# Optimization experiments

Hardware: AMD Instinct MI355X
Metric: run time of the kernel (lower is better)

## Reference

```python
import jax, jax.numpy as jnp
import numpy as np

NUM_HEADS = 8
GRAPH_DIM = 64
K_RATIO = 0.1
SIM_THRESH = 0.6


def _gat_layer(h_in, mask, W, a_src, a_dst, b):
    # PyG GATConv (heads=1, eval mode): lin (no bias), alpha = LeakyReLU(a_src.h_j + a_dst.h_i),
    # softmax over source nodes j per target i (edges given by dense mask, self loops included), + bias.
    h = h_in @ W                                   # [N, F]
    asrc = h @ a_src                               # [N] source term
    adst = h @ a_dst                               # [N] target term
    logits = jax.nn.leaky_relu(adst[:, None] + asrc[None, :], 0.2)  # [target i, source j]
    logits = jnp.where(mask.T, logits, -1e30)      # mask[j,i]: edge src j -> dst i (symmetric here)
    alpha = jax.nn.softmax(logits, axis=-1)
    return alpha @ h + b


def _forward(x, w_qkv, w_proj, b_proj, gat0_W, gat0_asrc, gat0_adst, gat0_b,
             gat1_W, gat1_asrc, gat1_adst, gat1_b, w_g2a, b_g2a):
    B, C, H, W = x.shape
    HW = H * W
    nh = NUM_HEADS
    hd = C // nh
    scale = hd ** -0.5
    x_seq = x.reshape(B, C, HW).transpose(0, 2, 1)                 # [B, HW, C]

    # ---- build_spatial_graph ----
    importance = jnp.var(x_seq, axis=-1, ddof=1)                   # torch.var default unbiased
    N = int(HW * K_RATIO)                                          # 102 nodes
    _, top_idx = jax.lax.top_k(importance, N)                      # [B, N]
    feats = jnp.take_along_axis(x_seq, top_idx[..., None], axis=1) # [B, N, C]
    fn = feats / jnp.clip(jnp.linalg.norm(feats, axis=-1, keepdims=True), 1e-12)
    sim = fn @ fn.transpose(0, 2, 1)                               # [B, N, N]
    adj = sim > SIM_THRESH
    adj = adj | jnp.eye(N, dtype=bool)                             # GATConv add_self_loops

    # ---- per-batch GAT stack + graph_to_attn ----
    def per_graph(f, m):
        g = jax.nn.relu(_gat_layer(f, m, gat0_W, gat0_asrc, gat0_adst, gat0_b))
        g = jax.nn.relu(_gat_layer(g, m, gat1_W, gat1_asrc, gat1_adst, gat1_b))
        return jax.nn.sigmoid(g @ w_g2a.T + b_g2a)                 # [N, nh]
    gw = jax.vmap(per_graph)(feats, adj)                           # [B, N, nh]

    # ---- dense multi-head attention ----
    qkv = (x_seq @ w_qkv.T).reshape(B, HW, 3, nh, hd).transpose(2, 0, 3, 1, 4)
    q, k, v = qkv[0], qkv[1], qkv[2]                               # [B, nh, HW, hd]
    scores = jnp.einsum('bhqd,bhkd->bhqk', q, k) * scale           # [B, nh, HW, HW]

    # ---- graph modulation scatter (replaces the nested python loops) ----
    vals = jnp.where(adj[..., None], gw[:, :, None, :] * gw[:, None, :, :], 0.0)  # [B, N, N, nh]
    gm = jnp.zeros_like(scores)
    bidx = jnp.arange(B)[:, None, None]
    gm = gm.at[bidx, :, top_idx[:, :, None], top_idx[:, None, :]].set(vals)
    scores = scores + gm

    attn = jax.nn.softmax(scores, axis=-1)                         # dropout is identity in eval
    out = jnp.einsum('bhqk,bhkd->bhqd', attn, v).transpose(0, 2, 1, 3).reshape(B, HW, C)
    out = out @ w_proj.T + b_proj
    return out.transpose(0, 2, 1).reshape(B, C, H, W)


def setup_inputs() -> dict:
    key = jax.random.key(0)
    ks = jax.random.split(key, 16)
    dim, gd, nh = 256, GRAPH_DIM, NUM_HEADS
    B, H, W = 8, 32, 32
    s = 0.02
    return {
        'x': jax.random.normal(ks[0], (B, dim, H, W), dtype=jnp.float32),
        'w_qkv': s * jax.random.normal(ks[1], (3 * dim, dim), dtype=jnp.float32),
        'w_proj': s * jax.random.normal(ks[2], (dim, dim), dtype=jnp.float32),
        'b_proj': jnp.zeros((dim,), dtype=jnp.float32),
        'gat0_W': s * jax.random.normal(ks[3], (dim, gd), dtype=jnp.float32),
        'gat0_asrc': s * jax.random.normal(ks[4], (gd,), dtype=jnp.float32),
        'gat0_adst': s * jax.random.normal(ks[5], (gd,), dtype=jnp.float32),
        'gat0_b': jnp.zeros((gd,), dtype=jnp.float32),
        'gat1_W': s * jax.random.normal(ks[6], (gd, gd), dtype=jnp.float32),
        'gat1_asrc': s * jax.random.normal(ks[7], (gd,), dtype=jnp.float32),
        'gat1_adst': s * jax.random.normal(ks[8], (gd,), dtype=jnp.float32),
        'gat1_b': jnp.zeros((gd,), dtype=jnp.float32),
        'w_g2a': s * jax.random.normal(ks[9], (nh, gd), dtype=jnp.float32),
        'b_g2a': jnp.zeros((nh,), dtype=jnp.float32),
    }


def reference(x, w_qkv, w_proj, b_proj, gat0_W, gat0_asrc, gat0_adst, gat0_b,
              gat1_W, gat1_asrc, gat1_adst, gat1_b, w_g2a, b_g2a):
    return _forward(x, w_qkv, w_proj, b_proj, gat0_W, gat0_asrc, gat0_adst, gat0_b,
                    gat1_W, gat1_asrc, gat1_adst, gat1_b, w_g2a, b_g2a)
```

## Files before the change

### kernel.cpp

```cpp
#include <hip/hip_runtime.h>
#include <math.h>

#define NB 8
#define CDIM 256
#define HWD 1024
#define NH 8
#define HD 32
#define NN 102
#define GD 64

typedef __attribute__((ext_vector_type(8))) short bf16x8;
typedef __attribute__((ext_vector_type(4))) float f32x4;

__device__ inline short f2bf(float f) {
  union { float f; unsigned u; } v; v.f = f;
  unsigned r = v.u + 0x7fffu + ((v.u >> 16) & 1u);
  return (short)(r >> 16);
}
__device__ inline float bf2f(short s) {
  union { unsigned u; float f; } v;
  v.u = ((unsigned)(unsigned short)s) << 16;
  return v.f;
}

__global__ __launch_bounds__(256) void wsplit_k(const float* __restrict__ w_qkv,
                                                const float* __restrict__ w_proj,
                                                short* __restrict__ wqh, short* __restrict__ wql,
                                                short* __restrict__ wph, short* __restrict__ wpl) {
  int t = blockIdx.x * 256 + threadIdx.x;
  if (t < 196608) {
    float v = w_qkv[t];
    short hi = f2bf(v);
    wqh[t] = hi; wql[t] = f2bf(v - bf2f(hi));
  } else {
    int u = t - 196608;
    float v = w_proj[u];
    short hi = f2bf(v);
    wph[u] = hi; wpl[u] = f2bf(v - bf2f(hi));
  }
}

__global__ __launch_bounds__(256) void xsplit_k(const float* __restrict__ x,
                                                short* __restrict__ xth,
                                                short* __restrict__ xtl) {
  __shared__ float tile[64][65];
  int p0 = blockIdx.x * 64, c0 = blockIdx.y * 64, b = blockIdx.z;
  int t = threadIdx.x;
  {
    int g = t >> 6, p = t & 63;
#pragma unroll
    for (int i = 0; i < 16; ++i) {
      int cc = g * 16 + i;
      tile[cc][p] = x[((size_t)(b * 256 + c0 + cc)) * 1024 + p0 + p];
    }
  }
  __syncthreads();
  {
    int p = t >> 2, cs = (t & 3) * 16;
    size_t rb = ((size_t)(b * 1024 + p0 + p)) * 256 + c0 + cs;
#pragma unroll
    for (int g = 0; g < 4; ++g) {
      short4 hv, lv;
      float f0 = tile[cs + g * 4 + 0][p];
      float f1 = tile[cs + g * 4 + 1][p];
      float f2 = tile[cs + g * 4 + 2][p];
      float f3 = tile[cs + g * 4 + 3][p];
      hv.x = f2bf(f0); lv.x = f2bf(f0 - bf2f(hv.x));
      hv.y = f2bf(f1); lv.y = f2bf(f1 - bf2f(hv.y));
      hv.z = f2bf(f2); lv.z = f2bf(f2 - bf2f(hv.z));
      hv.w = f2bf(f3); lv.w = f2bf(f3 - bf2f(hv.w));
      *(short4*)(xth + rb + g * 4) = hv;
      *(short4*)(xtl + rb + g * 4) = lv;
    }
  }
}

__global__ __launch_bounds__(256) void prep_k(const float* __restrict__ g0W,
                                              const float* __restrict__ g1W,
                                              short* __restrict__ w0bT,
                                              short* __restrict__ w1bT) {
  int t = blockIdx.x * 256 + threadIdx.x;
  if (t < 16384) {
    int c = t >> 6, f = t & 63;
    w0bT[f * 256 + c] = f2bf(g0W[t]);
  } else if (t < 20480) {
    int u2 = t - 16384;
    int c = u2 >> 6, f = u2 & 63;
    w1bT[f * 64 + c] = f2bf(g1W[u2]);
  }
}

__global__ __launch_bounds__(256) void importance_k(const float* __restrict__ x,
                                                    float* __restrict__ imp) {
  __shared__ float red[8][33];
  int bp = blockIdx.x;
  int b = bp >> 5, p0 = (bp & 31) << 5;
  int t = threadIdx.x;
  int pl = t & 31, cg = t >> 5;
  const float* xp = x + (size_t)b * CDIM * HWD + p0 + pl;
  float s = 0.f;
  for (int cc = 0; cc < 32; ++cc) s += xp[(size_t)(cg * 32 + cc) * HWD];
  red[cg][pl] = s;
  __syncthreads();
  float tot = 0.f;
  for (int g = 0; g < 8; ++g) tot += red[g][pl];
  float mean = tot * (1.f / CDIM);
  __syncthreads();
  float v = 0.f;
  for (int cc = 0; cc < 32; ++cc) {
    float d = xp[(size_t)(cg * 32 + cc) * HWD] - mean;
    v += d * d;
  }
  red[cg][pl] = v;
  __syncthreads();
  if (t < 32) {
    float vv = 0.f;
    for (int g = 0; g < 8; ++g) vv += red[g][t];
    imp[b * 1024 + p0 + t] = vv * (1.f / (CDIM - 1));
  }
}

union GraphLDS {
  struct { float sv[1024]; int si[1024]; } tk;
  struct {
    short h0T[64 * 136];
    short alphaB[102 * 136];
    short gB[102 * 72];
  } m;
};

__global__ __launch_bounds__(1024) void graph_k(
    const float* __restrict__ x, const float* __restrict__ imp,
    const short* __restrict__ w0bT, const short* __restrict__ w1bT,
    const float* __restrict__ g0as, const float* __restrict__ g0ad,
    const float* __restrict__ g0b,
    const float* __restrict__ g1as, const float* __restrict__ g1ad,
    const float* __restrict__ g1b,
    const float* __restrict__ wg2a, const float* __restrict__ bg2a,
    int* __restrict__ nodeof, short* __restrict__ fnG,
    unsigned char* __restrict__ adjG, float* __restrict__ gwb) {
  __shared__ GraphLDS u;
  __shared__ ushort adjPack[NN][8];
  __shared__ float normL[NN];
  __shared__ float asrcL[NN], adstL[NN];
  __shared__ int topiL[NN];
  int b = blockIdx.x, t = threadIdx.x;
  int wv = t >> 6, lane = t & 63, quad = lane >> 4, l16 = lane & 15;

  u.tk.sv[t] = imp[b * 1024 + t];
  u.tk.si[t] = t;
  nodeof[b * 1024 + t] = -1;
  __syncthreads();
  for (int k = 2; k <= 1024; k <<= 1) {
    for (int j = k >> 1; j > 0; j >>= 1) {
      int ixj = t ^ j;
      if (ixj > t) {
        bool up = ((t & k) == 0);
        float a = u.tk.sv[t], c = u.tk.sv[ixj];
        if ((a > c) == up) {
          u.tk.sv[t] = c; u.tk.sv[ixj] = a;
          int ti = u.tk.si[t]; u.tk.si[t] = u.tk.si[ixj]; u.tk.si[ixj] = ti;
        }
      }
      __syncthreads();
    }
  }
  if (t >= 1024 - NN) {
    int n = 1023 - t;
    int idx = u.tk.si[t];
    topiL[n] = idx;
    nodeof[b * 1024 + idx] = n;
  }
  __syncthreads();

  {
    int n = t >> 3, g = t & 7;
    if (n < NN) {
      int idx = topiL[n];
      const float* xb = x + (size_t)b * CDIM * HWD + idx;
      float vbuf[32];
      float ssl = 0.f;
#pragma unroll
      for (int cc = 0; cc < 32; ++cc) {
        float v = xb[(size_t)(g * 32 + cc) * HWD];
        vbuf[cc] = v;
        ssl += v * v;
      }
      ssl += __shfl_xor(ssl, 1);
      ssl += __shfl_xor(ssl, 2);
      ssl += __shfl_xor(ssl, 4);
      float nrm = sqrtf(ssl);
      float rn = 1.f / fmaxf(nrm, 1e-12f);
      if (g == 0) normL[n] = nrm;
      short* fp = fnG + ((size_t)b * 112 + n) * 256 + g * 32;
#pragma unroll
      for (int cc = 0; cc < 32; cc += 4) {
        short4 s4 = {f2bf(vbuf[cc] * rn), f2bf(vbuf[cc + 1] * rn),
                     f2bf(vbuf[cc + 2] * rn), f2bf(vbuf[cc + 3] * rn)};
        *(short4*)(fp + cc) = s4;
      }
    }
  }
  for (int e = t; e < 64 * 34; e += 1024) {
    int f = e / 34, c = 102 + (e % 34);
    u.m.h0T[f * 136 + c] = 0;
  }
  __syncthreads();

  for (int tile = wv; tile < 49; tile += 16) {
    int I = tile / 7, J = tile % 7;
    const short* ap = fnG + ((size_t)b * 112 + I * 16 + l16) * 256 + quad * 8;
    const short* bp = fnG + ((size_t)b * 112 + J * 16 + l16) * 256 + quad * 8;
    f32x4 acc = (f32x4){0.f, 0.f, 0.f, 0.f};
#pragma unroll
    for (int kb = 0; kb < 8; ++kb)
      acc = __builtin_amdgcn_mfma_f32_16x16x32_bf16(*(const bf16x8*)(ap + kb * 32),
                                                    *(const bf16x8*)(bp + kb * 32), acc, 0, 0, 0);
#pragma unroll
    for (int r = 0; r < 4; ++r) {
      int i = I * 16 + quad * 4 + r, j = J * 16 + l16;
      bool e = (acc[r] > 0.6f) || (i == j);
      unsigned long long m = __ballot(e);
      if (l16 == 0) {
        int row = I * 16 + quad * 4 + r;
        if (row < NN) adjPack[row][J] = (ushort)((m >> (quad * 16)) & 0xFFFFull);
      }
      if (i < NN && j < NN) adjG[(size_t)b * NN * NN + i * NN + j] = e ? 1 : 0;
    }
  }
  __syncthreads();

  for (int tile = wv; tile < 28; tile += 16) {
    int mt = tile >> 2, nt = tile & 3;
    const short* ap = fnG + ((size_t)b * 112 + mt * 16 + l16) * 256 + quad * 8;
    const short* bp = w0bT + (nt * 16 + l16) * 256 + quad * 8;
    f32x4 acc = (f32x4){0.f, 0.f, 0.f, 0.f};
#pragma unroll
    for (int kb = 0; kb < 8; ++kb)
      acc = __builtin_amdgcn_mfma_f32_16x16x32_bf16(*(const bf16x8*)(ap + kb * 32),
                                                    *(const bf16x8*)(bp + kb * 32), acc, 0, 0, 0);
    int f = nt * 16 + l16;
#pragma unroll
    for (int r = 0; r < 4; ++r) {
      int node = mt * 16 + quad * 4 + r;
      if (node < NN) u.m.h0T[f * 136 + node] = f2bf(acc[r] * normL[node]);
    }
  }
  __syncthreads();

  for (int layer = 0; layer < 2; ++layer) {
    const float* avs = layer ? g1as : g0as;
    const float* avd = layer ? g1ad : g0ad;
    const float* bias = layer ? g1b : g0b;
    {
      int n = t >> 3, g = t & 7;
      if (n < NN) {
        float s1 = 0.f, s2 = 0.f;
#pragma unroll
        for (int uu = 0; uu < 8; ++uu) {
          int f = g * 8 + uu;
          float hv = bf2f(u.m.h0T[f * 136 + n]);
          s1 += hv * avs[f];
          s2 += hv * avd[f];
        }
        s1 += __shfl_xor(s1, 1); s1 += __shfl_xor(s1, 2); s1 += __shfl_xor(s1, 4);
        s2 += __shfl_xor(s2, 1); s2 += __shfl_xor(s2, 2); s2 += __shfl_xor(s2, 4);
        if (g == 0) { asrcL[n] = s1; adstL[n] = s2; }
      }
    }
    __syncthreads();
    for (int i = wv; i < NN; i += 16) {
      float zi = adstL[i];
      int j1 = 64 + lane;
      bool e0 = (adjPack[i][lane >> 4] >> (lane & 15)) & 1;
      bool e1 = (j1 < NN) && ((adjPack[i][j1 >> 4] >> (j1 & 15)) & 1);
      float p0 = 0.f, p1 = 0.f;
      if (e0) { float z = zi + asrcL[lane]; p0 = __expf(z > 0.f ? z : 0.2f * z); }
      if (e1) { float z = zi + asrcL[j1]; p1 = __expf(z > 0.f ? z : 0.2f * z); }
      float s = p0 + p1;
      s += __shfl_xor(s, 1); s += __shfl_xor(s, 2); s += __shfl_xor(s, 4);
      s += __shfl_xor(s, 8); s += __shfl_xor(s, 16); s += __shfl_xor(s, 32);
      float inv = 1.f / s;
      u.m.alphaB[i * 136 + lane] = f2bf(p0 * inv);
      u.m.alphaB[i * 136 + 64 + lane] = f2bf(p1 * inv);
    }
    __syncthreads();
    for (int tile = wv; tile < 28; tile += 16) {
      int mt = tile >> 2, nt = tile & 3;
      int ar = mt * 16 + l16; if (ar > NN - 1) ar = NN - 1;
      const short* ap = &u.m.alphaB[ar * 136 + quad * 8];
      const short* bp = &u.m.h0T[(nt * 16 + l16) * 136 + quad * 8];
      f32x4 acc = (f32x4){0.f, 0.f, 0.f, 0.f};
#pragma unroll
      for (int kb = 0; kb < 4; ++kb)
        acc = __builtin_amdgcn_mfma_f32_16x16x32_bf16(*(const bf16x8*)(ap + kb * 32),
                                                      *(const bf16x8*)(bp + kb * 32), acc, 0, 0, 0);
      int f = nt * 16 + l16;
      float bv = bias[f];
#pragma unroll
      for (int r = 0; r < 4; ++r) {
        int i = mt * 16 + quad * 4 + r;
        if (i < NN) u.m.gB[i * 72 + f] = f2bf(fmaxf(acc[r] + bv, 0.f));
      }
    }
    __syncthreads();
    if (layer == 0) {
      for (int tile = wv; tile < 28; tile += 16) {
        int mt = tile >> 2, nt = tile & 3;
        int ar = mt * 16 + l16; if (ar > NN - 1) ar = NN - 1;
        const short* ap = &u.m.gB[ar * 72 + quad * 8];
        const short* bp = w1bT + (nt * 16 + l16) * 64 + quad * 8;
        f32x4 acc = (f32x4){0.f, 0.f, 0.f, 0.f};
#pragma unroll
        for (int kb = 0; kb < 2; ++kb)
          acc = __builtin_amdgcn_mfma_f32_16x16x32_bf16(*(const bf16x8*)(ap + kb * 32),
                                                        *(const bf16x8*)(bp + kb * 32), acc, 0, 0, 0);
        int f = nt * 16 + l16;
#pragma unroll
        for (int r = 0; r < 4; ++r) {
          int node = mt * 16 + quad * 4 + r;
          if (node < NN) u.m.h0T[f * 136 + node] = f2bf(acc[r]);
        }
      }
      __syncthreads();
    }
  }
  float* wgL = (float*)&u.m.alphaB[0];
  if (t < 512) wgL[t] = wg2a[t];
  __syncthreads();
  if (t < NN * NH) {
    int n = t >> 3, h = t & 7;
    float z = bg2a[h];
#pragma unroll
    for (int c = 0; c < GD; ++c) z += bf2f(u.m.gB[n * 72 + c]) * wgL[h * 64 + c];
    gwb[((size_t)b * NN + n) * NH + h] = 1.f / (1.f + __expf(-z));
  }
}

__global__ __launch_bounds__(256) void qkv_k(const short* __restrict__ xth,
                                             const short* __restrict__ xtl,
                                             const short* __restrict__ wqh,
                                             const short* __restrict__ wql,
                                             short* __restrict__ qhp, short* __restrict__ qlp,
                                             short* __restrict__ khp, short* __restrict__ klp,
                                             short* __restrict__ vtp) {
  __shared__ short vs_s[4][64 * 24];
  int t = threadIdx.x, wid = t >> 6, lane = t & 63, quad = lane >> 4, l16 = lane & 15;
  int m0 = blockIdx.x * 64, y = blockIdx.y;
  int b = m0 >> 10;
  int row = m0 + wid * 16 + l16;
  int p_base = (m0 & 1023) + wid * 16;
  int qi = y >> 2, n0 = (y & 3) * 64;
  const short* wh = wqh + (size_t)(qi * 256 + n0) * 256;
  const short* wl = wql + (size_t)(qi * 256 + n0) * 256;
  const short* arh = xth + (size_t)row * 256 + quad * 8;
  const short* arl = xtl + (size_t)row * 256 + quad * 8;
  f32x4 acc[4];
#pragma unroll
  for (int nt = 0; nt < 4; ++nt) acc[nt] = (f32x4){0.f, 0.f, 0.f, 0.f};
#pragma unroll
  for (int kb = 0; kb < 8; ++kb) {
    bf16x8 ah = *(const bf16x8*)(arh + kb * 32);
    bf16x8 al = *(const bf16x8*)(arl + kb * 32);
#pragma unroll
    for (int nt = 0; nt < 4; ++nt) {
      size_t wo = (size_t)(nt * 16 + l16) * 256 + kb * 32 + quad * 8;
      bf16x8 bh_ = *(const bf16x8*)(wh + wo);
      bf16x8 bl_ = *(const bf16x8*)(wl + wo);
      acc[nt] = __builtin_amdgcn_mfma_f32_16x16x32_bf16(ah, bh_, acc[nt], 0, 0, 0);
      acc[nt] = __builtin_amdgcn_mfma_f32_16x16x32_bf16(ah, bl_, acc[nt], 0, 0, 0);
      acc[nt] = __builtin_amdgcn_mfma_f32_16x16x32_bf16(al, bh_, acc[nt], 0, 0, 0);
    }
  }
  if (qi < 2) {
    const float scale = (qi == 0) ? 0.17677669529663687f : 1.f;
    short* hp = (qi == 0) ? qhp : khp;
    short* lp = (qi == 0) ? qlp : klp;
#pragma unroll
    for (int nt = 0; nt < 4; ++nt) {
      int nq = n0 + nt * 16 + l16;
      int h = nq >> 5, d = nq & 31;
#pragma unroll
      for (int r = 0; r < 4; ++r) {
        int p = p_base + quad * 4 + r;
        float v = acc[nt][r] * scale;
        short hi = f2bf(v);
        short lo = f2bf(v - bf2f(hi));
        size_t e = ((size_t)(b * 8 + h) * 1024 + p) * 32 + d;
        hp[e] = hi;
        lp[e] = lo;
      }
    }
  } else {
    short* vs = &vs_s[wid][0];
#pragma unroll
    for (int nt = 0; nt < 4; ++nt)
#pragma unroll
      for (int r = 0; r < 4; ++r)
        vs[(nt * 16 + l16) * 24 + quad * 4 + r] = f2bf(acc[nt][r]);
    int nq = n0 + lane;
    int h = nq >> 5, d = nq & 31;
    size_t rb = ((size_t)(b * 8 + h) * 32 + d) * 1024 + p_base;
    *(bf16x8*)(vtp + rb) = *(const bf16x8*)(vs + lane * 24);
    *(bf16x8*)(vtp + rb + 8) = *(const bf16x8*)(vs + lane * 24 + 8);
  }
}

__global__ __launch_bounds__(256, 4) void attn_k(const short* __restrict__ qh,
                                                 const short* __restrict__ ql,
                                                 const short* __restrict__ kh,
                                                 const short* __restrict__ kl,
                                                 const short* __restrict__ vt,
                                                 const int* __restrict__ nodeof,
                                                 const float* __restrict__ gw,
                                                 const unsigned char* __restrict__ adj,
                                                 short* __restrict__ aoh,
                                                 short* __restrict__ aol) {
  __shared__ __align__(16) short p_s[4][16 * 72];
  __shared__ float aw_s[4][16];
  int t = threadIdx.x;
  int wid = t >> 6, lane = t & 63, quad = lane >> 4, l16 = lane & 15;
  int bh = blockIdx.x, b = bh >> 3, h = bh & 7;
  int q0 = blockIdx.y * 64 + wid * 16;
  size_t base = (size_t)bh * 32768;
  short* pw = &p_s[wid][0];
  float* aw = &aw_s[wid][0];

  size_t qoff = base + (size_t)(q0 + l16) * 32 + quad * 8;
  bf16x8 qhf = *(const bf16x8*)(qh + qoff);
  bf16x8 qlf = *(const bf16x8*)(ql + qoff);

  int irow[4]; float grq[4];
#pragma unroll
  for (int r = 0; r < 4; ++r) {
    int qr = q0 + quad * 4 + r;
    int in_ = nodeof[b * 1024 + qr];
    irow[r] = in_;
    grq[r] = (in_ >= 0) ? gw[((size_t)b * NN + in_) * NH + h] : 0.f;
  }
  const unsigned char* adjB = adj + (size_t)b * NN * NN;

  f32x4 ot[2];
  ot[0] = (f32x4){0.f, 0.f, 0.f, 0.f};
  ot[1] = (f32x4){0.f, 0.f, 0.f, 0.f};
  float l_r[4] = {0.f, 0.f, 0.f, 0.f};

  for (int ch = 0; ch < 16; ++ch) {
    int c0 = ch * 64;
    bf16x8 khf[4], klf[4];
#pragma unroll
    for (int ni = 0; ni < 4; ++ni) {
      size_t off = base + (size_t)(c0 + ni * 16 + l16) * 32 + quad * 8;
      khf[ni] = *(const bf16x8*)(kh + off);
      klf[ni] = *(const bf16x8*)(kl + off);
    }
    bf16x8 vaf[2][2];
#pragma unroll
    for (int mi = 0; mi < 2; ++mi)
#pragma unroll
      for (int ks = 0; ks < 2; ++ks)
        vaf[mi][ks] = *(const bf16x8*)(vt + base + (size_t)(mi * 16 + l16) * 1024 +
                                       c0 + ks * 32 + quad * 8);
    int jn[4]; float gcn[4];
#pragma unroll
    for (int ni = 0; ni < 4; ++ni) {
      int j = nodeof[b * 1024 + c0 + ni * 16 + l16];
      jn[ni] = j;
      gcn[ni] = (j >= 0) ? gw[((size_t)b * NN + j) * NH + h] : 0.f;
    }
    f32x4 s[4];
#pragma unroll
    for (int ni = 0; ni < 4; ++ni) {
      f32x4 a = (f32x4){0.f, 0.f, 0.f, 0.f};
      a = __builtin_amdgcn_mfma_f32_16x16x32_bf16(qhf, khf[ni], a, 0, 0, 0);
      a = __builtin_amdgcn_mfma_f32_16x16x32_bf16(qhf, klf[ni], a, 0, 0, 0);
      a = __builtin_amdgcn_mfma_f32_16x16x32_bf16(qlf, khf[ni], a, 0, 0, 0);
      s[ni] = a;
    }
#pragma unroll
    for (int r = 0; r < 4; ++r) {
      int in_ = irow[r];
      if (in_ >= 0) {
        const unsigned char* ar = adjB + (size_t)in_ * NN;
        float g = grq[r];
#pragma unroll
        for (int ni = 0; ni < 4; ++ni)
          if (jn[ni] >= 0 && ar[jn[ni]]) s[ni][r] += g * gcn[ni];
      }
    }
#pragma unroll
    for (int r = 0; r < 4; ++r) {
      float e0 = __expf(s[0][r]);
      float e1 = __expf(s[1][r]);
      float e2 = __expf(s[2][r]);
      float e3 = __expf(s[3][r]);
      l_r[r] += (e0 + e1) + (e2 + e3);
      int prow = (quad * 4 + r) * 72;
      pw[prow + 0 + l16] = f2bf(e0);
      pw[prow + 16 + l16] = f2bf(e1);
      pw[prow + 32 + l16] = f2bf(e2);
      pw[prow + 48 + l16] = f2bf(e3);
    }
#pragma unroll
    for (int ks = 0; ks < 2; ++ks) {
      bf16x8 pb = *(const bf16x8*)(pw + l16 * 72 + ks * 32 + quad * 8);
      ot[0] = __builtin_amdgcn_mfma_f32_16x16x32_bf16(vaf[0][ks], pb, ot[0], 0, 0, 0);
      ot[1] = __builtin_amdgcn_mfma_f32_16x16x32_bf16(vaf[1][ks], pb, ot[1], 0, 0, 0);
    }
  }
#pragma unroll
  for (int r = 0; r < 4; ++r) {
    float ls = l_r[r];
    ls += __shfl_xor(ls, 1);
    ls += __shfl_xor(ls, 2);
    ls += __shfl_xor(ls, 4);
    ls += __shfl_xor(ls, 8);
    if (l16 == 0) aw[quad * 4 + r] = 1.f / ls;
  }
  float li = aw[l16];
  ot[0] *= li;
  ot[1] *= li;
  float* os = (float*)pw;
#pragma unroll
  for (int mi = 0; mi < 2; ++mi)
#pragma unroll
    for (int r = 0; r < 4; ++r)
      os[l16 * 36 + mi * 16 + quad * 4 + r] = ot[mi][r];
  int qr2 = lane >> 2, dg = (lane & 3) * 8;
  float f[8];
  *(float4*)&f[0] = *(float4*)&os[qr2 * 36 + dg];
  *(float4*)&f[4] = *(float4*)&os[qr2 * 36 + dg + 4];
  bf16x8 hv, lv;
#pragma unroll
  for (int j = 0; j < 8; ++j) {
    hv[j] = f2bf(f[j]);
    lv[j] = f2bf(f[j] - bf2f(hv[j]));
  }
  size_t ob = (size_t)(b * 1024 + q0 + qr2) * 256 + h * 32 + dg;
  *(bf16x8*)(aoh + ob) = hv;
  *(bf16x8*)(aol + ob) = lv;
}

__global__ __launch_bounds__(256) void proj_k(const short* __restrict__ aoh,
                                              const short* __restrict__ aol,
                                              const short* __restrict__ wph,
                                              const short* __restrict__ wpl,
                                              const float* __restrict__ bias,
                                              float* __restrict__ out) {
  __shared__ float os_s[4][64 * 20];
  int t = threadIdx.x, wid = t >> 6, lane = t & 63, quad = lane >> 4, l16 = lane & 15;
  int m0 = blockIdx.x * 64, n0 = blockIdx.y * 64;
  int b = m0 >> 10;
  int row = m0 + wid * 16 + l16;
  int p_base = (m0 & 1023) + wid * 16;
  const short* arh = aoh + (size_t)row * 256 + quad * 8;
  const short* arl = aol + (size_t)row * 256 + quad * 8;
  f32x4 acc[4];
#pragma unroll
  for (int nt = 0; nt < 4; ++nt) acc[nt] = (f32x4){0.f, 0.f, 0.f, 0.f};
#pragma unroll
  for (int kb = 0; kb < 8; ++kb) {
    bf16x8 ah = *(const bf16x8*)(arh + kb * 32);
    bf16x8 al = *(const bf16x8*)(arl + kb * 32);
#pragma unroll
    for (int nt = 0; nt < 4; ++nt) {
      size_t wo = (size_t)(n0 + nt * 16 + l16) * 256 + kb * 32 + quad * 8;
      bf16x8 bh_ = *(const bf16x8*)(wph + wo);
      bf16x8 bl_ = *(const bf16x8*)(wpl + wo);
      acc[nt] = __builtin_amdgcn_mfma_f32_16x16x32_bf16(ah, bh_, acc[nt], 0, 0, 0);
      acc[nt] = __builtin_amdgcn_mfma_f32_16x16x32_bf16(ah, bl_, acc[nt], 0, 0, 0);
      acc[nt] = __builtin_amdgcn_mfma_f32_16x16x32_bf16(al, bh_, acc[nt], 0, 0, 0);
    }
  }
  float* os = &os_s[wid][0];
#pragma unroll
  for (int nt = 0; nt < 4; ++nt) {
    float bv = bias[n0 + nt * 16 + l16];
#pragma unroll
    for (int r = 0; r < 4; ++r)
      os[(nt * 16 + l16) * 20 + quad * 4 + r] = acc[nt][r] + bv;
  }
  int c = n0 + lane;
  float* orow = out + ((size_t)(b * 256 + c)) * 1024 + p_base;
#pragma unroll
  for (int g = 0; g < 4; ++g)
    *(float4*)(orow + g * 4) = *(float4*)&os[lane * 20 + g * 4];
}

extern "C" void kernel_launch(void* const* d_in, const int* in_sizes, int n_in,
                              void* d_out, int out_size, void* d_ws, size_t ws_size,
                              hipStream_t stream) {
  const float* x      = (const float*)d_in[0];
  const float* w_qkv  = (const float*)d_in[1];
  const float* w_proj = (const float*)d_in[2];
  const float* b_proj = (const float*)d_in[3];
  const float* g0W    = (const float*)d_in[4];
  const float* g0as   = (const float*)d_in[5];
  const float* g0ad   = (const float*)d_in[6];
  const float* g0b    = (const float*)d_in[7];
  const float* g1W    = (const float*)d_in[8];
  const float* g1as   = (const float*)d_in[9];
  const float* g1ad   = (const float*)d_in[10];
  const float* g1b    = (const float*)d_in[11];
  const float* wg2a   = (const float*)d_in[12];
  const float* bg2a   = (const float*)d_in[13];
  float* out = (float*)d_out;
  float* ws = (float*)d_ws;

  size_t o = 0;
  auto alloc = [&](size_t nf) { float* p = ws + o; o += (nf + 15) & ~(size_t)15; return p; };
  float* imp    = alloc(8 * 1024);
  int*   nodeof = (int*)alloc(8 * 1024);
  short* fnG    = (short*)alloc(8 * 112 * 256 / 2);
  short* w0bT   = (short*)alloc(256 * 64 / 2);
  short* w1bT   = (short*)alloc(64 * 64 / 2);
  unsigned char* adj = (unsigned char*)alloc((8 * NN * NN + 3) / 4 + 16);
  float* gwb    = alloc(8 * NN * 8);
  short* xth    = (short*)alloc(1048576);
  short* xtl    = (short*)alloc(1048576);
  short* wqh    = (short*)alloc(98304);
  short* wql    = (short*)alloc(98304);
  short* wph    = (short*)alloc(32768);
  short* wpl    = (short*)alloc(32768);
  short* qh     = (short*)alloc(1048576);
  short* ql     = (short*)alloc(1048576);
  short* kh     = (short*)alloc(1048576);
  short* kl     = (short*)alloc(1048576);
  short* vt     = (short*)alloc(1048576);
  short* aoh    = (short*)alloc(1048576);
  short* aol    = (short*)alloc(1048576);
  if (ws_size < o * sizeof(float)) return;

  importance_k<<<256, 256, 0, stream>>>(x, imp);
  wsplit_k<<<1024, 256, 0, stream>>>(w_qkv, w_proj, wqh, wql, wph, wpl);
  xsplit_k<<<dim3(16, 4, 8), 256, 0, stream>>>(x, xth, xtl);
  prep_k<<<80, 256, 0, stream>>>(g0W, g1W, w0bT, w1bT);
  graph_k<<<8, 1024, 0, stream>>>(x, imp, w0bT, w1bT, g0as, g0ad, g0b,
                                  g1as, g1ad, g1b, wg2a, bg2a,
                                  nodeof, fnG, adj, gwb);
  qkv_k<<<dim3(128, 12), 256, 0, stream>>>(xth, xtl, wqh, wql, qh, ql, kh, kl, vt);
  attn_k<<<dim3(64, 16), 256, 0, stream>>>(qh, ql, kh, kl, vt, nodeof, gwb, adj, aoh, aol);
  proj_k<<<dim3(128, 4), 256, 0, stream>>>(aoh, aol, wph, wpl, b_proj, out);
}
```

Baseline: 356.1 us.

## Split attention over key halves with a reduce pass, halve GEMM output tiles

The attention kernel now splits each query tile's key range into two halves on a third grid dimension. Each half writes unnormalized partial outputs and row sums to fp32 scratch, and a new reduce kernel combines them, normalizes, and produces the hi/lo bf16 split. The QKV and projection GEMMs use 32-wide output tiles instead of 64-wide, doubling block count, and several kernels get a higher occupancy launch bound. The goal is more blocks to fill the GPU, at the cost of an extra launch, scratch traffic, and less reuse of the A operand in the GEMMs.

```diff
diff --git a/kernel.cpp b/kernel.cpp
--- a/kernel.cpp
+++ b/kernel.cpp
@@ -337,33 +337,33 @@
   }
 }
 
-__global__ __launch_bounds__(256) void qkv_k(const short* __restrict__ xth,
-                                             const short* __restrict__ xtl,
-                                             const short* __restrict__ wqh,
-                                             const short* __restrict__ wql,
-                                             short* __restrict__ qhp, short* __restrict__ qlp,
-                                             short* __restrict__ khp, short* __restrict__ klp,
-                                             short* __restrict__ vtp) {
-  __shared__ short vs_s[4][64 * 24];
+__global__ __launch_bounds__(256, 8) void qkv_k(const short* __restrict__ xth,
+                                                const short* __restrict__ xtl,
+                                                const short* __restrict__ wqh,
+                                                const short* __restrict__ wql,
+                                                short* __restrict__ qhp, short* __restrict__ qlp,
+                                                short* __restrict__ khp, short* __restrict__ klp,
+                                                short* __restrict__ vtp) {
+  __shared__ short vs_s[4][32 * 24];
   int t = threadIdx.x, wid = t >> 6, lane = t & 63, quad = lane >> 4, l16 = lane & 15;
   int m0 = blockIdx.x * 64, y = blockIdx.y;
   int b = m0 >> 10;
   int row = m0 + wid * 16 + l16;
   int p_base = (m0 & 1023) + wid * 16;
-  int qi = y >> 2, n0 = (y & 3) * 64;
-  const short* wh = wqh + (size_t)(qi * 256 + n0) * 256;
-  const short* wl = wql + (size_t)(qi * 256 + n0) * 256;
+  int qi = y >> 3, n0 = (y & 7) * 32;
+  const short* wh = wqh + ((size_t)qi * 256 + n0) * 256;
+  const short* wl = wql + ((size_t)qi * 256 + n0) * 256;
   const short* arh = xth + (size_t)row * 256 + quad * 8;
   const short* arl = xtl + (size_t)row * 256 + quad * 8;
-  f32x4 acc[4];
-#pragma unroll
-  for (int nt = 0; nt < 4; ++nt) acc[nt] = (f32x4){0.f, 0.f, 0.f, 0.f};
+  f32x4 acc[2];
+  acc[0] = (f32x4){0.f, 0.f, 0.f, 0.f};
+  acc[1] = (f32x4){0.f, 0.f, 0.f, 0.f};
 #pragma unroll
   for (int kb = 0; kb < 8; ++kb) {
     bf16x8 ah = *(const bf16x8*)(arh + kb * 32);
     bf16x8 al = *(const bf16x8*)(arl + kb * 32);
 #pragma unroll
-    for (int nt = 0; nt < 4; ++nt) {
+    for (int nt = 0; nt < 2; ++nt) {
       size_t wo = (size_t)(nt * 16 + l16) * 256 + kb * 32 + quad * 8;
       bf16x8 bh_ = *(const bf16x8*)(wh + wo);
       bf16x8 bl_ = *(const bf16x8*)(wl + wo);
@@ -377,7 +377,7 @@
     short* hp = (qi == 0) ? qhp : khp;
     short* lp = (qi == 0) ? qlp : klp;
 #pragma unroll
-    for (int nt = 0; nt < 4; ++nt) {
+    for (int nt = 0; nt < 2; ++nt) {
       int nq = n0 + nt * 16 + l16;
       int h = nq >> 5, d = nq & 31;
 #pragma unroll
@@ -394,19 +394,19 @@
   } else {
     short* vs = &vs_s[wid][0];
 #pragma unroll
-    for (int nt = 0; nt < 4; ++nt)
+    for (int nt = 0; nt < 2; ++nt)
 #pragma unroll
       for (int r = 0; r < 4; ++r)
         vs[(nt * 16 + l16) * 24 + quad * 4 + r] = f2bf(acc[nt][r]);
-    int nq = n0 + lane;
+    int cl = lane >> 1, hf = lane & 1;
+    int nq = n0 + cl;
     int h = nq >> 5, d = nq & 31;
-    size_t rb = ((size_t)(b * 8 + h) * 32 + d) * 1024 + p_base;
-    *(bf16x8*)(vtp + rb) = *(const bf16x8*)(vs + lane * 24);
-    *(bf16x8*)(vtp + rb + 8) = *(const bf16x8*)(vs + lane * 24 + 8);
-  }
-}
-
-__global__ __launch_bounds__(256, 4) void attn_k(const short* __restrict__ qh,
+    size_t rb = ((size_t)(b * 8 + h) * 32 + d) * 1024 + p_base + hf * 8;
+    *(bf16x8*)(vtp + rb) = *(const bf16x8*)(vs + cl * 24 + hf * 8);
+  }
+}
+
+__global__ __launch_bounds__(256, 8) void attn_k(const short* __restrict__ qh,
                                                  const short* __restrict__ ql,
                                                  const short* __restrict__ kh,
                                                  const short* __restrict__ kl,
@@ -414,14 +414,15 @@
                                                  const int* __restrict__ nodeof,
                                                  const float* __restrict__ gw,
                                                  const unsigned char* __restrict__ adj,
-                                                 short* __restrict__ aoh,
-                                                 short* __restrict__ aol) {
+                                                 float* __restrict__ po,
+                                                 float* __restrict__ pl) {
   __shared__ __align__(16) short p_s[4][16 * 72];
   __shared__ float aw_s[4][16];
   int t = threadIdx.x;
   int wid = t >> 6, lane = t & 63, quad = lane >> 4, l16 = lane & 15;
   int bh = blockIdx.x, b = bh >> 3, h = bh & 7;
-  int q0 = blockIdx.y * 64 + wid * 16;
+  int qt = blockIdx.y, khalf = blockIdx.z;
+  int q0 = qt * 64 + wid * 16;
   size_t base = (size_t)bh * 32768;
   short* pw = &p_s[wid][0];
   float* aw = &aw_s[wid][0];
@@ -445,7 +446,7 @@
   ot[1] = (f32x4){0.f, 0.f, 0.f, 0.f};
   float l_r[4] = {0.f, 0.f, 0.f, 0.f};
 
-  for (int ch = 0; ch < 16; ++ch) {
+  for (int ch = khalf * 8; ch < khalf * 8 + 8; ++ch) {
     int c0 = ch * 64;
     bf16x8 khf[4], klf[4];
 #pragma unroll
@@ -515,55 +516,77 @@
     ls += __shfl_xor(ls, 2);
     ls += __shfl_xor(ls, 4);
     ls += __shfl_xor(ls, 8);
-    if (l16 == 0) aw[quad * 4 + r] = 1.f / ls;
-  }
-  float li = aw[l16];
-  ot[0] *= li;
-  ot[1] *= li;
+    if (l16 == 0) aw[quad * 4 + r] = ls;
+  }
   float* os = (float*)pw;
 #pragma unroll
   for (int mi = 0; mi < 2; ++mi)
 #pragma unroll
     for (int r = 0; r < 4; ++r)
       os[l16 * 36 + mi * 16 + quad * 4 + r] = ot[mi][r];
+  int bht = bh * 16 + qt;
+  size_t pob = (((size_t)bht * 2 + khalf) * 64 + wid * 16) * 32;
   int qr2 = lane >> 2, dg = (lane & 3) * 8;
-  float f[8];
-  *(float4*)&f[0] = *(float4*)&os[qr2 * 36 + dg];
-  *(float4*)&f[4] = *(float4*)&os[qr2 * 36 + dg + 4];
+  *(float4*)&po[pob + qr2 * 32 + dg] = *(float4*)&os[qr2 * 36 + dg];
+  *(float4*)&po[pob + qr2 * 32 + dg + 4] = *(float4*)&os[qr2 * 36 + dg + 4];
+  if (lane < 16) pl[((size_t)bht * 2 + khalf) * 64 + wid * 16 + lane] = aw[lane];
+}
+
+__global__ __launch_bounds__(256) void reduce_k(const float* __restrict__ po,
+                                                const float* __restrict__ pl,
+                                                short* __restrict__ aoh,
+                                                short* __restrict__ aol) {
+  int bht = blockIdx.x;
+  int bh = bht >> 4, qt = bht & 15;
+  int b = bh >> 3, h = bh & 7;
+  int t = threadIdx.x;
+  int q = t >> 2, dg = (t & 3) * 8;
+  size_t b0 = (((size_t)bht * 2 + 0) * 64 + q) * 32 + dg;
+  size_t b1 = (((size_t)bht * 2 + 1) * 64 + q) * 32 + dg;
+  float4 a0 = *(const float4*)&po[b0];
+  float4 a1 = *(const float4*)&po[b0 + 4];
+  float4 c0 = *(const float4*)&po[b1];
+  float4 c1 = *(const float4*)&po[b1 + 4];
+  float l = pl[((size_t)bht * 2) * 64 + q] + pl[((size_t)bht * 2 + 1) * 64 + q];
+  float inv = 1.f / l;
+  float f[8] = {(a0.x + c0.x) * inv, (a0.y + c0.y) * inv,
+                (a0.z + c0.z) * inv, (a0.w + c0.w) * inv,
+                (a1.x + c1.x) * inv, (a1.y + c1.y) * inv,
+                (a1.z + c1.z) * inv, (a1.w + c1.w) * inv};
   bf16x8 hv, lv;
 #pragma unroll
   for (int j = 0; j < 8; ++j) {
     hv[j] = f2bf(f[j]);
     lv[j] = f2bf(f[j] - bf2f(hv[j]));
   }
-  size_t ob = (size_t)(b * 1024 + q0 + qr2) * 256 + h * 32 + dg;
+  size_t ob = (size_t)(b * 1024 + qt * 64 + q) * 256 + h * 32 + dg;
   *(bf16x8*)(aoh + ob) = hv;
   *(bf16x8*)(aol + ob) = lv;
 }
 
-__global__ __launch_bounds__(256) void proj_k(const short* __restrict__ aoh,
-                                              const short* __restrict__ aol,
-                                              const short* __restrict__ wph,
-                                              const short* __restrict__ wpl,
-                                              const float* __restrict__ bias,
-                                              float* __restrict__ out) {
-  __shared__ float os_s[4][64 * 20];
+__global__ __launch_bounds__(256, 8) void proj_k(const short* __restrict__ aoh,
+                                                 const short* __restrict__ aol,
+                                                 const short* __restrict__ wph,
+                                                 const short* __restrict__ wpl,
+                                                 const float* __restrict__ bias,
+                                                 float* __restrict__ out) {
+  __shared__ float os_s[4][32 * 20];
   int t = threadIdx.x, wid = t >> 6, lane = t & 63, quad = lane >> 4, l16 = lane & 15;
-  int m0 = blockIdx.x * 64, n0 = blockIdx.y * 64;
+  int m0 = blockIdx.x * 64, n0 = blockIdx.y * 32;
   int b = m0 >> 10;
   int row = m0 + wid * 16 + l16;
   int p_base = (m0 & 1023) + wid * 16;
   const short* arh = aoh + (size_t)row * 256 + quad * 8;
   const short* arl = aol + (size_t)row * 256 + quad * 8;
-  f32x4 acc[4];
-#pragma unroll
-  for (int nt = 0; nt < 4; ++nt) acc[nt] = (f32x4){0.f, 0.f, 0.f, 0.f};
+  f32x4 acc[2];
+  acc[0] = (f32x4){0.f, 0.f, 0.f, 0.f};
+  acc[1] = (f32x4){0.f, 0.f, 0.f, 0.f};
 #pragma unroll
   for (int kb = 0; kb < 8; ++kb) {
     bf16x8 ah = *(const bf16x8*)(arh + kb * 32);
     bf16x8 al = *(const bf16x8*)(arl + kb * 32);
 #pragma unroll
-    for (int nt = 0; nt < 4; ++nt) {
+    for (int nt = 0; nt < 2; ++nt) {
       size_t wo = (size_t)(n0 + nt * 16 + l16) * 256 + kb * 32 + quad * 8;
       bf16x8 bh_ = *(const bf16x8*)(wph + wo);
       bf16x8 bl_ = *(const bf16x8*)(wpl + wo);
@@ -574,17 +597,17 @@
   }
   float* os = &os_s[wid][0];
 #pragma unroll
-  for (int nt = 0; nt < 4; ++nt) {
+  for (int nt = 0; nt < 2; ++nt) {
     float bv = bias[n0 + nt * 16 + l16];
 #pragma unroll
     for (int r = 0; r < 4; ++r)
       os[(nt * 16 + l16) * 20 + quad * 4 + r] = acc[nt][r] + bv;
   }
-  int c = n0 + lane;
+  int cl = lane >> 1, hf = lane & 1;
+  int c = n0 + cl;
   float* orow = out + ((size_t)(b * 256 + c)) * 1024 + p_base;
-#pragma unroll
-  for (int g = 0; g < 4; ++g)
-    *(float4*)(orow + g * 4) = *(float4*)&os[lane * 20 + g * 4];
+  *(float4*)(orow + hf * 8) = *(float4*)&os[cl * 20 + hf * 8];
+  *(float4*)(orow + hf * 8 + 4) = *(float4*)&os[cl * 20 + hf * 8 + 4];
 }
 
 extern "C" void kernel_launch(void* const* d_in, const int* in_sizes, int n_in,
@@ -629,6 +652,8 @@
   short* vt     = (short*)alloc(1048576);
   short* aoh    = (short*)alloc(1048576);
   short* aol    = (short*)alloc(1048576);
+  float* po     = alloc((size_t)1024 * 2 * 64 * 32);
+  float* plv    = alloc((size_t)1024 * 2 * 64);
   if (ws_size < o * sizeof(float)) return;
 
   importance_k<<<256, 256, 0, stream>>>(x, imp);
@@ -638,7 +663,8 @@
   graph_k<<<8, 1024, 0, stream>>>(x, imp, w0bT, w1bT, g0as, g0ad, g0b,
                                   g1as, g1ad, g1b, wg2a, bg2a,
                                   nodeof, fnG, adj, gwb);
-  qkv_k<<<dim3(128, 12), 256, 0, stream>>>(xth, xtl, wqh, wql, qh, ql, kh, kl, vt);
-  attn_k<<<dim3(64, 16), 256, 0, stream>>>(qh, ql, kh, kl, vt, nodeof, gwb, adj, aoh, aol);
-  proj_k<<<dim3(128, 4), 256, 0, stream>>>(aoh, aol, wph, wpl, b_proj, out);
-}
+  qkv_k<<<dim3(128, 24), 256, 0, stream>>>(xth, xtl, wqh, wql, qh, ql, kh, kl, vt);
+  attn_k<<<dim3(64, 16, 2), 256, 0, stream>>>(qh, ql, kh, kl, vt, nodeof, gwb, adj, po, plv);
+  reduce_k<<<1024, 256, 0, stream>>>(po, plv, aoh, aol);
+  proj_k<<<dim3(128, 8), 256, 0, stream>>>(aoh, aol, wph, wpl, b_proj, out);
+}
```

New measurement: 464.7 us. 30.5% more time.
